# Kernel tuning notes

Measured on AMD Instinct MI355X. Metric: run time of the kernel, lower is better.

Reference implementation:

```python
import jax, jax.numpy as jnp
import numpy as np

D_MODEL = 1024
NUM_HEADS = 16


def setup_inputs() -> dict:
    key = jax.random.key(0)
    ks = jax.random.split(key, 6)
    B, N, L, C = 16, 1024, 120, D_MODEL
    s = 0.02
    return {
        "x": jax.random.normal(ks[0], (B, N, C), jnp.float32),
        "cond": jax.random.normal(ks[1], (B, L, C), jnp.float32),
        "mask": jax.random.randint(ks[2], (B, L), 0, 2, jnp.int32),
        "Wq": jax.random.normal(ks[3], (C, C), jnp.float32) * s,
        "bq": jnp.zeros((C,), jnp.float32),
        "Wkv": jax.random.normal(ks[4], (2 * C, C), jnp.float32) * s,
        "bkv": jnp.zeros((2 * C,), jnp.float32),
        "Wp": jax.random.normal(ks[5], (C, C), jnp.float32) * s,
        "bp": jnp.zeros((C,), jnp.float32),
    }


def reference(x, cond, mask, Wq, bq, Wkv, bkv, Wp, bp):
    B, N, C = x.shape
    H = NUM_HEADS
    Dh = C // H
    scale = Dh ** (-0.5)
    # q: (B,H,N,Dh)
    q = (x @ Wq.T + bq).reshape(B, N, H, Dh).transpose(0, 2, 1, 3)
    # kv: (2,B,H,L,Dh)
    L = cond.shape[1]
    kv = (cond @ Wkv.T + bkv).reshape(B, L, 2, H, Dh).transpose(2, 0, 3, 1, 4)
    k, v = kv[0], kv[1]
    # attention scores (B,H,N,L)
    attn = jnp.einsum("bhnd,bhld->bhnl", q, k) * scale
    attn = jnp.where(mask[:, None, None, :] == 0, -jnp.inf, attn)
    attn = jax.nn.softmax(attn, axis=-1)
    out = jnp.einsum("bhnl,bhld->bhnd", attn, v)  # (B,H,N,Dh)
    out = out.transpose(0, 2, 1, 3).reshape(B, N, C)
    return out @ Wp.T + bp
```

## Files before the change

kernel.cpp:

```cpp
#include <hip/hip_runtime.h>

typedef unsigned short u16;
typedef unsigned int u32;
typedef float f32x4 __attribute__((ext_vector_type(4)));
typedef __bf16 bf16x8 __attribute__((ext_vector_type(8)));
typedef u32 u32x4 __attribute__((ext_vector_type(4)));
typedef u16 u16x4 __attribute__((ext_vector_type(4)));

#define NB 16
#define NSEQ 1024
#define NL 120
#define NLP 128
#define NC 1024
#define NH 16
#define NDH 64

__device__ __forceinline__ u16 f2bf(float f) {
  u32 u = __float_as_uint(f);
  return (u16)((u + 0x7fffu + ((u >> 16) & 1u)) >> 16);
}

__device__ __forceinline__ void gld_lds16(const void* g, void* l) {
  __builtin_amdgcn_global_load_lds(
      (const __attribute__((address_space(1))) void*)g,
      (__attribute__((address_space(3))) void*)l, 16, 0, 0);
}

__global__ __launch_bounds__(256) void cast_all(
    const float* __restrict__ x, u16* __restrict__ xb,
    const float* __restrict__ cond, u16* __restrict__ condb,
    const float* __restrict__ Wq, u16* __restrict__ Wqb,
    const float* __restrict__ Wkv, u16* __restrict__ Wkvb,
    const float* __restrict__ Wp, u16* __restrict__ Wpb) {
  int bk = blockIdx.x;
  const float* src;
  u16* dst;
  if (bk < 16384) { src = x; dst = xb; }
  else if (bk < 18304) { src = cond; dst = condb; bk -= 16384; }
  else if (bk < 19328) { src = Wq; dst = Wqb; bk -= 18304; }
  else if (bk < 21376) { src = Wkv; dst = Wkvb; bk -= 19328; }
  else { src = Wp; dst = Wpb; bk -= 21376; }
  size_t i = ((size_t)bk * 256 + threadIdx.x) * 4;
  f32x4 v = *(const f32x4*)(src + i);
  u16x4 o;
  o.x = f2bf(v.x); o.y = f2bf(v.y); o.z = f2bf(v.z); o.w = f2bf(v.w);
  *(u16x4*)(dst + i) = o;
}

template <bool OUT_F32>
__global__ __launch_bounds__(256) void gemm_bt(
    const u16* __restrict__ A, const u16* __restrict__ Bt,
    const float* __restrict__ bias, void* __restrict__ Cout,
    int M, int Nn, int K) {
  __shared__ u16 As[128 * 32];
  __shared__ u16 Bs[128 * 32];
  const int mt = M >> 7;
  const int bm = (int)blockIdx.x % mt;
  const int bn = (int)blockIdx.x / mt;
  const int m0 = bm << 7, n0 = bn << 7;
  const int tid = threadIdx.x;
  const int w = tid >> 6, lane = tid & 63;
  const int wm = (w & 1) << 6, wn = (w >> 1) << 6;
  const int quad = lane >> 4, l15 = lane & 15;

  f32x4 acc[4][4];
#pragma unroll
  for (int i = 0; i < 4; ++i)
#pragma unroll
    for (int j = 0; j < 4; ++j) acc[i][j] = (f32x4){0.f, 0.f, 0.f, 0.f};

  const int r0 = tid >> 2;
  const int cb = (tid & 3) << 3;
  const u16* aP = A + (size_t)(m0 + r0) * K + cb;
  const u16* bP = Bt + (size_t)(n0 + r0) * K + cb;
  u16* asDst = &As[r0 * 32 + cb];
  u16* bsDst = &Bs[r0 * 32 + cb];

  for (int k0 = 0; k0 < K; k0 += 32) {
    __syncthreads();
    gld_lds16(aP + k0, asDst);
    gld_lds16(aP + (size_t)64 * K + k0, asDst + 64 * 32);
    gld_lds16(bP + k0, bsDst);
    gld_lds16(bP + (size_t)64 * K + k0, bsDst + 64 * 32);
    __syncthreads();

    bf16x8 af[4], bfr[4];
#pragma unroll
    for (int i = 0; i < 4; ++i)
      af[i] = *(const bf16x8*)&As[(wm + i * 16 + l15) * 32 + quad * 8];
#pragma unroll
    for (int j = 0; j < 4; ++j)
      bfr[j] = *(const bf16x8*)&Bs[(wn + j * 16 + l15) * 32 + quad * 8];
#pragma unroll
    for (int i = 0; i < 4; ++i)
#pragma unroll
      for (int j = 0; j < 4; ++j)
        acc[i][j] =
            __builtin_amdgcn_mfma_f32_16x16x32_bf16(af[i], bfr[j], acc[i][j], 0, 0, 0);
  }

#pragma unroll
  for (int j = 0; j < 4; ++j) {
    const int col = n0 + wn + j * 16 + l15;
    const float bv = bias[col];
#pragma unroll
    for (int i = 0; i < 4; ++i) {
      const int row = m0 + wm + i * 16 + quad * 4;
#pragma unroll
      for (int r = 0; r < 4; ++r) {
        const float v = acc[i][j][r] + bv;
        if (OUT_F32)
          ((float*)Cout)[(size_t)(row + r) * Nn + col] = v;
        else
          ((u16*)Cout)[(size_t)(row + r) * Nn + col] = f2bf(v);
      }
    }
  }
}

__global__ __launch_bounds__(256) void attn(
    const u16* __restrict__ Qb, const u16* __restrict__ KVb,
    const int* __restrict__ mask, u16* __restrict__ Ob) {
  __shared__ u16 Ks[NLP * NDH];
  __shared__ u16 Vt[NDH * NLP];
  __shared__ float mb[NLP];
  __shared__ u16 pb[4][16 * NLP];

  const int chunk = (int)blockIdx.x & 3;
  const int h = ((int)blockIdx.x >> 2) & 15;
  const int b = (int)blockIdx.x >> 6;
  const int tid = threadIdx.x;
  const int w = tid >> 6, lane = tid & 63;
  const int quad = lane >> 4, l15 = lane & 15;
  const u16* kvbase = KVb + (size_t)b * NL * 2 * NC;

  for (int i = tid; i < NLP * 8; i += 256) {
    const int l = i >> 3, c8 = (i & 7) * 8;
    u32x4 z = {0u, 0u, 0u, 0u};
    u32x4 v = (l < NL) ? *(const u32x4*)(kvbase + (size_t)l * 2 * NC + h * NDH + c8) : z;
    *(u32x4*)&Ks[l * NDH + c8] = v;
  }
  u16* vstage = &pb[0][0];
  for (int i = tid; i < NL * 8; i += 256) {
    const int l = i >> 3, c8 = (i & 7) * 8;
    *(u32x4*)&vstage[l * NDH + c8] =
        *(const u32x4*)(kvbase + (size_t)l * 2 * NC + NC + h * NDH + c8);
  }
  for (int i = tid; i < NLP; i += 256)
    mb[i] = (i < NL && mask[b * NL + i] != 0) ? 0.0f : -1e30f;
  __syncthreads();
  for (int i = tid; i < NDH * NLP; i += 256) {
    const int d = i >> 7, l = i & 127;
    Vt[d * NLP + l] = (l < NL) ? vstage[l * NDH + d] : (u16)0;
  }
  __syncthreads();

  const float scale = 0.125f;
  for (int it = 0; it < 4; ++it) {
    const int q0 = chunk * 256 + it * 64 + w * 16;
    const u16* qptr = Qb + (size_t)(b * NSEQ + q0 + l15) * NC + h * NDH + quad * 8;
    const bf16x8 a0 = *(const bf16x8*)qptr;
    const bf16x8 a1 = *(const bf16x8*)(qptr + 32);

    f32x4 s[8];
#pragma unroll
    for (int kt = 0; kt < 8; ++kt) {
      const u16* kb = &Ks[(kt * 16 + l15) * NDH + quad * 8];
      const bf16x8 b0 = *(const bf16x8*)kb;
      const bf16x8 b1 = *(const bf16x8*)(kb + 32);
      f32x4 t = {0.f, 0.f, 0.f, 0.f};
      t = __builtin_amdgcn_mfma_f32_16x16x32_bf16(a0, b0, t, 0, 0, 0);
      t = __builtin_amdgcn_mfma_f32_16x16x32_bf16(a1, b1, t, 0, 0, 0);
      s[kt] = t;
    }
#pragma unroll
    for (int kt = 0; kt < 8; ++kt) {
      const float mbv = mb[kt * 16 + l15];
#pragma unroll
      for (int r = 0; r < 4; ++r) s[kt][r] = s[kt][r] * scale + mbv;
    }
    float sum[4];
#pragma unroll
    for (int r = 0; r < 4; ++r) {
      float m = s[0][r];
#pragma unroll
      for (int kt = 1; kt < 8; ++kt) m = fmaxf(m, s[kt][r]);
      m = fmaxf(m, __shfl_xor(m, 1));
      m = fmaxf(m, __shfl_xor(m, 2));
      m = fmaxf(m, __shfl_xor(m, 4));
      m = fmaxf(m, __shfl_xor(m, 8));
      float su = 0.f;
#pragma unroll
      for (int kt = 0; kt < 8; ++kt) {
        s[kt][r] = __expf(s[kt][r] - m);
        su += s[kt][r];
      }
      su += __shfl_xor(su, 1);
      su += __shfl_xor(su, 2);
      su += __shfl_xor(su, 4);
      su += __shfl_xor(su, 8);
      sum[r] = su;
    }
#pragma unroll
    for (int r = 0; r < 4; ++r) {
      const float inv = 1.0f / sum[r];
#pragma unroll
      for (int kt = 0; kt < 8; ++kt)
        pb[w][(quad * 4 + r) * NLP + kt * 16 + l15] = f2bf(s[kt][r] * inv);
    }
#pragma unroll
    for (int ntl = 0; ntl < 4; ++ntl) {
      f32x4 o = {0.f, 0.f, 0.f, 0.f};
#pragma unroll
      for (int kt = 0; kt < 4; ++kt) {
        const bf16x8 pa = *(const bf16x8*)&pb[w][l15 * NLP + kt * 32 + quad * 8];
        const bf16x8 vb = *(const bf16x8*)&Vt[(ntl * 16 + l15) * NLP + kt * 32 + quad * 8];
        o = __builtin_amdgcn_mfma_f32_16x16x32_bf16(pa, vb, o, 0, 0, 0);
      }
#pragma unroll
      for (int r = 0; r < 4; ++r)
        Ob[(size_t)(b * NSEQ + q0 + quad * 4 + r) * NC + h * NDH + ntl * 16 + l15] =
            f2bf(o[r]);
    }
  }
}

extern "C" void kernel_launch(void* const* d_in, const int* in_sizes, int n_in,
                              void* d_out, int out_size, void* d_ws, size_t ws_size,
                              hipStream_t stream) {
  const float* x = (const float*)d_in[0];
  const float* cond = (const float*)d_in[1];
  const int* mask = (const int*)d_in[2];
  const float* Wq = (const float*)d_in[3];
  const float* bq = (const float*)d_in[4];
  const float* Wkv = (const float*)d_in[5];
  const float* bkv = (const float*)d_in[6];
  const float* Wp = (const float*)d_in[7];
  const float* bp = (const float*)d_in[8];

  char* ws = (char*)d_ws;
  u16* xb = (u16*)(ws + 0);
  u16* condb = (u16*)(ws + 33554432);
  u16* Wqb = (u16*)(ws + 37486592);
  u16* Wkvb = (u16*)(ws + 39583744);
  u16* Wpb = (u16*)(ws + 43778048);
  u16* Qb = (u16*)(ws + 45875200);
  u16* KVb = (u16*)(ws + 79429632);
  u16* Ob = xb;

  cast_all<<<22400, 256, 0, stream>>>(x, xb, cond, condb, Wq, Wqb, Wkv, Wkvb, Wp, Wpb);

  gemm_bt<false><<<128 * 8, 256, 0, stream>>>(xb, Wqb, bq, Qb, 16384, 1024, 1024);
  gemm_bt<false><<<15 * 16, 256, 0, stream>>>(condb, Wkvb, bkv, KVb, 1920, 2048, 1024);
  attn<<<1024, 256, 0, stream>>>(Qb, KVb, mask, Ob);
  gemm_bt<true><<<128 * 8, 256, 0, stream>>>(Ob, Wpb, bp, d_out, 16384, 1024, 1024);
}
```

Baseline: 331.6 us.

## Replace LDS-staged GEMM with direct-global 32x32x16 MFMA loads

The GEMM no longer stages A and B tiles through shared memory with barriers. Each wave now loads its bf16 fragments straight from global memory and uses 32x32x16 MFMA instructions with 2x2 accumulator tiles, and an occupancy hint is added to launch bounds. This removes the LDS round trip and the __syncthreads per k-step. In exchange, waves sharing a block re-read the same A and B rows from global memory or cache with no shared reuse, and the per-lane loads are strided by K, which may cost bandwidth and latency.

After: 470.1 us. 41.8% more time.

```diff
diff --git a/kernel.cpp b/kernel.cpp
--- a/kernel.cpp
+++ b/kernel.cpp
@@ -3,6 +3,7 @@
 typedef unsigned short u16;
 typedef unsigned int u32;
 typedef float f32x4 __attribute__((ext_vector_type(4)));
+typedef float f32x16 __attribute__((ext_vector_type(16)));
 typedef __bf16 bf16x8 __attribute__((ext_vector_type(8)));
 typedef u32 u32x4 __attribute__((ext_vector_type(4)));
 typedef u16 u16x4 __attribute__((ext_vector_type(4)));
@@ -18,12 +19,6 @@
 __device__ __forceinline__ u16 f2bf(float f) {
   u32 u = __float_as_uint(f);
   return (u16)((u + 0x7fffu + ((u >> 16) & 1u)) >> 16);
-}
-
-__device__ __forceinline__ void gld_lds16(const void* g, void* l) {
-  __builtin_amdgcn_global_load_lds(
-      (const __attribute__((address_space(1))) void*)g,
-      (__attribute__((address_space(3))) void*)l, 16, 0, 0);
 }
 
 __global__ __launch_bounds__(256) void cast_all(
@@ -48,12 +43,10 @@
 }
 
 template <bool OUT_F32>
-__global__ __launch_bounds__(256) void gemm_bt(
+__global__ __launch_bounds__(256, 4) void gemm_dg(
     const u16* __restrict__ A, const u16* __restrict__ Bt,
     const float* __restrict__ bias, void* __restrict__ Cout,
     int M, int Nn, int K) {
-  __shared__ u16 As[128 * 32];
-  __shared__ u16 Bs[128 * 32];
   const int mt = M >> 7;
   const int bm = (int)blockIdx.x % mt;
   const int bn = (int)blockIdx.x / mt;
@@ -61,58 +54,57 @@
   const int tid = threadIdx.x;
   const int w = tid >> 6, lane = tid & 63;
   const int wm = (w & 1) << 6, wn = (w >> 1) << 6;
-  const int quad = lane >> 4, l15 = lane & 15;
-
-  f32x4 acc[4][4];
-#pragma unroll
-  for (int i = 0; i < 4; ++i)
-#pragma unroll
-    for (int j = 0; j < 4; ++j) acc[i][j] = (f32x4){0.f, 0.f, 0.f, 0.f};
-
-  const int r0 = tid >> 2;
-  const int cb = (tid & 3) << 3;
-  const u16* aP = A + (size_t)(m0 + r0) * K + cb;
-  const u16* bP = Bt + (size_t)(n0 + r0) * K + cb;
-  u16* asDst = &As[r0 * 32 + cb];
-  u16* bsDst = &Bs[r0 * 32 + cb];
+  const int l31 = lane & 31, hl = lane >> 5;
+
+  const u16* aB = A + (size_t)(m0 + wm + l31) * K + hl * 8;
+  const u16* bB = Bt + (size_t)(n0 + wn + l31) * K + hl * 8;
+  const size_t rs32 = (size_t)32 * K;
+
+  f32x16 acc[2][2];
+#pragma unroll
+  for (int i = 0; i < 2; ++i)
+#pragma unroll
+    for (int j = 0; j < 2; ++j)
+#pragma unroll
+      for (int r = 0; r < 16; ++r) acc[i][j][r] = 0.f;
 
   for (int k0 = 0; k0 < K; k0 += 32) {
-    __syncthreads();
-    gld_lds16(aP + k0, asDst);
-    gld_lds16(aP + (size_t)64 * K + k0, asDst + 64 * 32);
-    gld_lds16(bP + k0, bsDst);
-    gld_lds16(bP + (size_t)64 * K + k0, bsDst + 64 * 32);
-    __syncthreads();
-
-    bf16x8 af[4], bfr[4];
-#pragma unroll
-    for (int i = 0; i < 4; ++i)
-      af[i] = *(const bf16x8*)&As[(wm + i * 16 + l15) * 32 + quad * 8];
-#pragma unroll
-    for (int j = 0; j < 4; ++j)
-      bfr[j] = *(const bf16x8*)&Bs[(wn + j * 16 + l15) * 32 + quad * 8];
-#pragma unroll
-    for (int i = 0; i < 4; ++i)
-#pragma unroll
-      for (int j = 0; j < 4; ++j)
-        acc[i][j] =
-            __builtin_amdgcn_mfma_f32_16x16x32_bf16(af[i], bfr[j], acc[i][j], 0, 0, 0);
-  }
-
-#pragma unroll
-  for (int j = 0; j < 4; ++j) {
-    const int col = n0 + wn + j * 16 + l15;
+    bf16x8 af[2][2], bf[2][2];
+#pragma unroll
+    for (int i = 0; i < 2; ++i)
+#pragma unroll
+      for (int ks = 0; ks < 2; ++ks)
+        af[i][ks] = *(const bf16x8*)(aB + i * rs32 + k0 + ks * 16);
+#pragma unroll
+    for (int j = 0; j < 2; ++j)
+#pragma unroll
+      for (int ks = 0; ks < 2; ++ks)
+        bf[j][ks] = *(const bf16x8*)(bB + j * rs32 + k0 + ks * 16);
+#pragma unroll
+    for (int ks = 0; ks < 2; ++ks)
+#pragma unroll
+      for (int i = 0; i < 2; ++i)
+#pragma unroll
+        for (int j = 0; j < 2; ++j)
+          acc[i][j] = __builtin_amdgcn_mfma_f32_32x32x16_bf16(af[i][ks], bf[j][ks],
+                                                              acc[i][j], 0, 0, 0);
+  }
+
+#pragma unroll
+  for (int j = 0; j < 2; ++j) {
+    const int col = n0 + wn + j * 32 + l31;
     const float bv = bias[col];
 #pragma unroll
-    for (int i = 0; i < 4; ++i) {
-      const int row = m0 + wm + i * 16 + quad * 4;
-#pragma unroll
-      for (int r = 0; r < 4; ++r) {
+    for (int i = 0; i < 2; ++i) {
+      const int rowb = m0 + wm + i * 32 + 4 * hl;
+#pragma unroll
+      for (int r = 0; r < 16; ++r) {
+        const int row = rowb + (r & 3) + 8 * (r >> 2);
         const float v = acc[i][j][r] + bv;
         if (OUT_F32)
-          ((float*)Cout)[(size_t)(row + r) * Nn + col] = v;
+          ((float*)Cout)[(size_t)row * Nn + col] = v;
         else
-          ((u16*)Cout)[(size_t)(row + r) * Nn + col] = f2bf(v);
+          ((u16*)Cout)[(size_t)row * Nn + col] = f2bf(v);
       }
     }
   }
@@ -250,8 +242,8 @@
 
   cast_all<<<22400, 256, 0, stream>>>(x, xb, cond, condb, Wq, Wqb, Wkv, Wkvb, Wp, Wpb);
 
-  gemm_bt<false><<<128 * 8, 256, 0, stream>>>(xb, Wqb, bq, Qb, 16384, 1024, 1024);
-  gemm_bt<false><<<15 * 16, 256, 0, stream>>>(condb, Wkvb, bkv, KVb, 1920, 2048, 1024);
+  gemm_dg<false><<<128 * 8, 256, 0, stream>>>(xb, Wqb, bq, Qb, 16384, 1024, 1024);
+  gemm_dg<false><<<15 * 16, 256, 0, stream>>>(condb, Wkvb, bkv, KVb, 1920, 2048, 1024);
   attn<<<1024, 256, 0, stream>>>(Qb, KVb, mask, Ob);
-  gemm_bt<true><<<128 * 8, 256, 0, stream>>>(Ob, Wpb, bp, d_out, 16384, 1024, 1024);
-}
+  gemm_dg<true><<<128 * 8, 256, 0, stream>>>(Ob, Wpb, bp, d_out, 16384, 1024, 1024);
+}
```
